# Performance work log

Measured on AMD Instinct MI355X. Metric: run time of the kernel, lower is better.

Reference implementation:

```python
import jax, jax.numpy as jnp
import numpy as np

N_NODE = 4096
N_BT = 4      # n_basis_time
N_BL = 4      # n_basis_loc (Chebyshev order)
WID = 5       # nn_width_basis_time
BATCH = 1048576
TAU_MAX = 10.0
T0, T1 = 0.0, 100.0


def sp100(z):
    # torch.nn.Softplus(beta=100): log(1+exp(100 z))/100
    return jax.nn.softplus(100.0 * z) / 100.0


def _mlp(t, W1, b1, W2, b2, W3, b3):
    # t: [B] scalar input per sample; params stacked over the n_basis_time axis n
    h = sp100(t[:, None, None] * W1[None, :, 0, :] + b1)        # [B, n, w]
    h = sp100(jnp.einsum('bnw,nwv->bnv', h, W2) + b2)           # [B, n, w]
    return (jnp.einsum('bnw,nwo->bno', h, W3) + b3)[..., 0]     # [B, n]


def setup_inputs() -> dict:
    key = jax.random.key(0)
    ks = jax.random.split(key, 18)
    tx = jax.random.uniform(ks[0], (BATCH,), minval=T0, maxval=T1)
    ty = jax.random.uniform(ks[1], (BATCH,), minval=T0, maxval=T1)
    xi = jax.random.randint(ks[2], (BATCH,), 0, N_NODE)
    yi = jax.random.randint(ks[3], (BATCH,), 0, N_NODE)
    x = jnp.stack([tx, xi.astype(jnp.float32)], axis=1)  # [B, 2]
    y = jnp.stack([ty, yi.astype(jnp.float32)], axis=1)  # [B, 2]
    # Stack of Chebyshev graph local filters (stand-in for precomputed T_k(L~))
    B = jax.random.normal(ks[4], (N_BL, N_NODE, N_NODE), dtype=jnp.float32) * 0.01
    g = 0.5  # init_gain-like scale
    inp = {'x': x, 'y': y, 'B': B}
    names = [('Wx1', (N_BT, 1, WID)), ('Wx2', (N_BT, WID, WID)), ('Wx3', (N_BT, WID, 1)),
             ('Wy1', (N_BT, 1, WID)), ('Wy2', (N_BT, WID, WID)), ('Wy3', (N_BT, WID, 1))]
    for i, (nm, shp) in enumerate(names):
        inp[nm] = jax.random.normal(ks[5 + i], shp, dtype=jnp.float32) * g
    inp['bx1'] = jnp.full((N_BT, WID), 0.1, jnp.float32)
    inp['bx2'] = jnp.full((N_BT, WID), 0.1, jnp.float32)
    inp['bx3'] = jnp.full((N_BT, 1), 0.1, jnp.float32)
    inp['by1'] = jnp.full((N_BT, WID), 0.1, jnp.float32)
    inp['by2'] = jnp.full((N_BT, WID), 0.1, jnp.float32)
    inp['by3'] = jnp.full((N_BT, 1), 0.1, jnp.float32)
    inp['W'] = jax.random.uniform(ks[11], (N_BT, N_BL), minval=-10.0, maxval=10.0)
    return inp


def reference(x, y, B, Wx1, Wx2, Wx3, Wy1, Wy2, Wy3,
              bx1, bx2, bx3, by1, by2, by3, W):
    dt = x[:, 0] - y[:, 0]                                  # [B]
    mask = (dt <= TAU_MAX).astype(x.dtype)                  # [B]
    scale = T1 - T0
    xb = _mlp(dt / scale, Wx1, bx1, Wx2, bx2, Wx3, bx3) * mask[:, None]   # [B, n_bt]
    yb = _mlp((y[:, 0] - T0) / scale, Wy1, by1, Wy2, by2, Wy3, by3)       # [B, n_bt]
    K_t = xb * yb                                           # [B, n_bt] (basis_dim=1 sum)
    xi = x[:, 1].astype(jnp.int32)
    yi = y[:, 1].astype(jnp.int32)
    K_l = B[:, yi, xi] * mask[None, :]                      # [n_bl, B] gather + mask-scatter
    # K[b] = sum_{i,j} K_t[b,i] * K_l[j,b] * W[i,j]
    return jnp.einsum('bi,jb,ij->b', K_t, K_l, W)
```

## Files before the change

### kernel.cpp

```cpp
#include <hip/hip_runtime.h>

#define N_NODE   4096
#define PLANE    (N_NODE * N_NODE)
#define TAU_MAX  10.0f
#define INV_SCALE 0.01f

__device__ __forceinline__ float sp100(float z) {
    float a = 100.0f * z;
    float e = __expf(-fabsf(a));
    return (fmaxf(a, 0.0f) + __logf(1.0f + e)) * 0.01f;
}

__device__ __forceinline__ float mlp_n(float t,
                                       const float* __restrict__ W1,
                                       const float* __restrict__ b1,
                                       const float* __restrict__ W2,
                                       const float* __restrict__ b2,
                                       const float* __restrict__ W3,
                                       const float* __restrict__ b3,
                                       int n) {
    float h1[5];
#pragma unroll
    for (int w = 0; w < 5; ++w)
        h1[w] = sp100(fmaf(t, W1[n * 5 + w], b1[n * 5 + w]));

    float h2[5];
#pragma unroll
    for (int v = 0; v < 5; ++v) {
        float acc = b2[n * 5 + v];
#pragma unroll
        for (int w = 0; w < 5; ++w)
            acc = fmaf(h1[w], W2[n * 25 + w * 5 + v], acc);
        h2[v] = sp100(acc);
    }

    float o = b3[n];
#pragma unroll
    for (int w = 0; w < 5; ++w)
        o = fmaf(h2[w], W3[n * 5 + w], o);
    return o;
}

__global__ __launch_bounds__(256)
void tdb_cheb_kernel(const float2* __restrict__ x,
                     const float2* __restrict__ y,
                     const float*  __restrict__ Bm,
                     const float*  __restrict__ Wx1, const float* __restrict__ Wx2,
                     const float*  __restrict__ Wx3,
                     const float*  __restrict__ Wy1, const float* __restrict__ Wy2,
                     const float*  __restrict__ Wy3,
                     const float*  __restrict__ bx1, const float* __restrict__ bx2,
                     const float*  __restrict__ bx3,
                     const float*  __restrict__ by1, const float* __restrict__ by2,
                     const float*  __restrict__ by3,
                     const float*  __restrict__ W,
                     float* __restrict__ out, int batch) {
    int b = blockIdx.x * blockDim.x + threadIdx.x;
    if (b >= batch) return;

    float2 xv = x[b];
    float2 yv = y[b];
    float dt = xv.x - yv.x;

    float res = 0.0f;
    if (dt <= TAU_MAX) {
        float tx = dt * INV_SCALE;
        float ty = yv.x * INV_SCALE;

        int xi = (int)xv.y;
        int yi = (int)yv.y;
        int idx = yi * N_NODE + xi;

        float kl0 = Bm[idx];
        float kl1 = Bm[idx + PLANE];
        float kl2 = Bm[idx + 2 * PLANE];
        float kl3 = Bm[idx + 3 * PLANE];

        float kt[4];
        for (int n = 0; n < 4; ++n) {
            float xb = mlp_n(tx, Wx1, bx1, Wx2, bx2, Wx3, bx3, n);
            float yb = mlp_n(ty, Wy1, by1, Wy2, by2, Wy3, by3, n);
            kt[n] = xb * yb;
        }

        float s0 = 0.f, s1 = 0.f, s2 = 0.f, s3 = 0.f;
#pragma unroll
        for (int i = 0; i < 4; ++i) {
            float k = kt[i];
            s0 = fmaf(k, W[i * 4 + 0], s0);
            s1 = fmaf(k, W[i * 4 + 1], s1);
            s2 = fmaf(k, W[i * 4 + 2], s2);
            s3 = fmaf(k, W[i * 4 + 3], s3);
        }
        res = fmaf(s0, kl0, fmaf(s1, kl1, fmaf(s2, kl2, s3 * kl3)));
    }
    out[b] = res;
}

extern "C" void kernel_launch(void* const* d_in, const int* in_sizes, int n_in,
                              void* d_out, int out_size, void* d_ws, size_t ws_size,
                              hipStream_t stream) {
    const float2* x   = (const float2*)d_in[0];
    const float2* y   = (const float2*)d_in[1];
    const float*  Bm  = (const float*)d_in[2];
    const float*  Wx1 = (const float*)d_in[3];
    const float*  Wx2 = (const float*)d_in[4];
    const float*  Wx3 = (const float*)d_in[5];
    const float*  Wy1 = (const float*)d_in[6];
    const float*  Wy2 = (const float*)d_in[7];
    const float*  Wy3 = (const float*)d_in[8];
    const float*  bx1 = (const float*)d_in[9];
    const float*  bx2 = (const float*)d_in[10];
    const float*  bx3 = (const float*)d_in[11];
    const float*  by1 = (const float*)d_in[12];
    const float*  by2 = (const float*)d_in[13];
    const float*  by3 = (const float*)d_in[14];
    const float*  W   = (const float*)d_in[15];
    float* out = (float*)d_out;

    int batch = in_sizes[0] / 2;
    int block = 256;
    int grid  = (batch + block - 1) / block;
    tdb_cheb_kernel<<<grid, block, 0, stream>>>(x, y, Bm,
                                                Wx1, Wx2, Wx3, Wy1, Wy2, Wy3,
                                                bx1, bx2, bx3, by1, by2, by3,
                                                W, out, batch);
}
```

Baseline: 387.7 us.

## Interleave Chebyshev planes into float4 layout before gathering

Adds a transpose kernel that rewrites the four B planes into one interleaved float4 array in the workspace, so the main kernel fetches all four filter values with a single 16-byte gather. The goal is to replace four scattered loads per sample with one. The transpose runs on every call and reads and writes the full 256 MB tensor, which adds a large fixed cost when the batch touches only a fraction of B. It also unrolls the per-basis MLP loop.

```diff
diff --git a/kernel.cpp b/kernel.cpp
--- a/kernel.cpp
+++ b/kernel.cpp
@@ -1,7 +1,7 @@
 #include <hip/hip_runtime.h>
 
 #define N_NODE   4096
-#define PLANE    (N_NODE * N_NODE)
+#define PLANE    ((size_t)N_NODE * N_NODE)
 #define TAU_MAX  10.0f
 #define INV_SCALE 0.01f
 
@@ -42,9 +42,25 @@
 }
 
 __global__ __launch_bounds__(256)
+void transpose_kernel(const float* __restrict__ Bm, float4* __restrict__ BT) {
+    size_t t  = (size_t)blockIdx.x * blockDim.x + threadIdx.x;
+    size_t p0 = t * 4;
+    float4 a = *(const float4*)(Bm + p0);
+    float4 b = *(const float4*)(Bm + PLANE + p0);
+    float4 c = *(const float4*)(Bm + 2 * PLANE + p0);
+    float4 d = *(const float4*)(Bm + 3 * PLANE + p0);
+    BT[p0 + 0] = make_float4(a.x, b.x, c.x, d.x);
+    BT[p0 + 1] = make_float4(a.y, b.y, c.y, d.y);
+    BT[p0 + 2] = make_float4(a.z, b.z, c.z, d.z);
+    BT[p0 + 3] = make_float4(a.w, b.w, c.w, d.w);
+}
+
+template <bool USE_BT>
+__global__ __launch_bounds__(256)
 void tdb_cheb_kernel(const float2* __restrict__ x,
                      const float2* __restrict__ y,
                      const float*  __restrict__ Bm,
+                     const float4* __restrict__ BT,
                      const float*  __restrict__ Wx1, const float* __restrict__ Wx2,
                      const float*  __restrict__ Wx3,
                      const float*  __restrict__ Wy1, const float* __restrict__ Wy2,
@@ -69,14 +85,21 @@
 
         int xi = (int)xv.y;
         int yi = (int)yv.y;
-        int idx = yi * N_NODE + xi;
+        size_t idx = (size_t)yi * N_NODE + xi;
 
-        float kl0 = Bm[idx];
-        float kl1 = Bm[idx + PLANE];
-        float kl2 = Bm[idx + 2 * PLANE];
-        float kl3 = Bm[idx + 3 * PLANE];
+        float kl0, kl1, kl2, kl3;
+        if (USE_BT) {
+            float4 kl = BT[idx];
+            kl0 = kl.x; kl1 = kl.y; kl2 = kl.z; kl3 = kl.w;
+        } else {
+            kl0 = Bm[idx];
+            kl1 = Bm[idx + PLANE];
+            kl2 = Bm[idx + 2 * PLANE];
+            kl3 = Bm[idx + 3 * PLANE];
+        }
 
         float kt[4];
+#pragma unroll
         for (int n = 0; n < 4; ++n) {
             float xb = mlp_n(tx, Wx1, bx1, Wx2, bx2, Wx3, bx3, n);
             float yb = mlp_n(ty, Wy1, by1, Wy2, by2, Wy3, by3, n);
@@ -121,8 +144,20 @@
     int batch = in_sizes[0] / 2;
     int block = 256;
     int grid  = (batch + block - 1) / block;
-    tdb_cheb_kernel<<<grid, block, 0, stream>>>(x, y, Bm,
-                                                Wx1, Wx2, Wx3, Wy1, Wy2, Wy3,
-                                                bx1, bx2, bx3, by1, by2, by3,
-                                                W, out, batch);
+
+    const size_t bt_bytes = PLANE * 4 * sizeof(float);
+    if (ws_size >= bt_bytes) {
+        float4* BT = (float4*)d_ws;
+        int tgrid = (int)(PLANE / 4 / 256);
+        transpose_kernel<<<tgrid, 256, 0, stream>>>(Bm, BT);
+        tdb_cheb_kernel<true><<<grid, block, 0, stream>>>(x, y, Bm, BT,
+                                                          Wx1, Wx2, Wx3, Wy1, Wy2, Wy3,
+                                                          bx1, bx2, bx3, by1, by2, by3,
+                                                          W, out, batch);
+    } else {
+        tdb_cheb_kernel<false><<<grid, block, 0, stream>>>(x, y, Bm, (const float4*)nullptr,
+                                                           Wx1, Wx2, Wx3, Wy1, Wy2, Wy3,
+                                                           bx1, bx2, bx3, by1, by2, by3,
+                                                           W, out, batch);
+    }
 }
```

Measured after the change: 496.9 us. 1.28x slower.
